# Performance work log

Hardware: AMD Instinct MI355X
Metric: run time of the kernel (lower is better)

The kernel has to match this reference:

```python
import jax, jax.numpy as jnp
import numpy as np

SCALE = 8
NUM_CLASSES = 15
IGNORE_THRES = 0.5
# anchors for scale=8 divided by scale
GRID_ANCHOR = jnp.array([[96.0 / 8, 230.0 / 8], [79.0 / 8, 186.0 / 8], [81.0 / 8, 133.0 / 8]], dtype=jnp.float32)  # [3,2]


def _bce_sum(p, t, mask):
    # torch BCELoss(reduction='sum') with log clamped at -100, restricted to mask
    lp = jnp.maximum(jnp.log(p), -100.0)
    ln = jnp.maximum(jnp.log(1.0 - p), -100.0)
    return jnp.sum(-(t * lp + (1.0 - t) * ln) * mask)


def setup_inputs() -> dict:
    key = jax.random.key(0)
    k1, k2, k3 = jax.random.split(key, 3)
    nB, nG = 128, 52
    x = jax.random.normal(k1, (nB, 3 * (NUM_CLASSES + 5), nG, nG), dtype=jnp.float32)
    boxes = jax.random.uniform(k2, (nB, 4), minval=0.1, maxval=0.6)  # cx,cy,w,h in (0,1)
    cls = jax.random.randint(k3, (nB, 1), 0, NUM_CLASSES).astype(jnp.float32)
    labels = jnp.concatenate([boxes, cls], axis=-1)  # [nB,5]
    return {"x": x, "labels": labels}


def reference(x, labels):
    nB, nG = x.shape[0], x.shape[2]
    pred = x.reshape(nB, 3, NUM_CLASSES + 5, nG, nG).transpose(0, 1, 3, 4, 2)  # [B,3,G,G,20]
    px = jax.nn.sigmoid(pred[..., 0])
    py = jax.nn.sigmoid(pred[..., 1])
    pw = pred[..., 2]
    ph = pred[..., 3]
    conf = jax.nn.sigmoid(pred[..., 4])
    cls = jax.nn.softmax(pred[..., 5:], axis=-1)
    pred_boxs = jnp.stack([px, py, pw, ph], axis=-1)  # [B,3,G,G,4]
    out = jnp.concatenate([
        pred_boxs.reshape(nB, -1, 4) * SCALE,
        conf.reshape(nB, -1, 1),
        cls.reshape(nB, -1, NUM_CLASSES),
    ], axis=-1)

    # ---- build_targets (vectorized; one target per image as in original loop) ----
    tb = labels[:, :4] * nG  # boxes in grid units [B,4]
    gx, gy, gw, gh = tb[:, 0], tb[:, 1], tb[:, 2], tb[:, 3]
    gi = gx.astype(jnp.int32)
    gj = gy.astype(jnp.int32)
    gcls = labels[:, 4].astype(jnp.int32)

    # wh-IoU anchors vs targets -> [3,B]
    aw, ah = GRID_ANCHOR[:, 0:1], GRID_ANCHOR[:, 1:2]
    inter_wh = jnp.minimum(aw, gw[None, :]) * jnp.minimum(ah, gh[None, :])
    ious = inter_wh / (aw * ah + 1e-16 + gw[None, :] * gh[None, :] - inter_wh)
    best_idx = jnp.argmax(ious, axis=0)  # [B]

    bidx = jnp.arange(nB)
    shape4 = (nB, 3, nG, nG)
    obj = jnp.zeros(shape4, jnp.float32).at[bidx, best_idx, gj, gi].set(1.0)

    noobj = jnp.ones(shape4, jnp.float32)
    arep = jnp.tile(jnp.arange(3), nB)
    brep = jnp.repeat(bidx, 3)
    jrep = jnp.repeat(gj, 3)
    irep = jnp.repeat(gi, 3)
    ign = (jnp.reshape(ious.T, (-1,)) > IGNORE_THRES).astype(jnp.float32)
    noobj = noobj.at[brep, arep, jrep, irep].mul(1.0 - ign)
    noobj = noobj.at[bidx, best_idx, gj, gi].set(0.0)

    gif = gi.astype(jnp.float32)
    gjf = gj.astype(jnp.float32)
    tx = jnp.zeros(shape4, jnp.float32).at[bidx, best_idx, gj, gi].set(gx - gif)
    ty = jnp.zeros(shape4, jnp.float32).at[bidx, best_idx, gj, gi].set(gy - gjf)
    tw = jnp.zeros(shape4, jnp.float32).at[bidx, best_idx, gj, gi].set(jnp.log(gw / GRID_ANCHOR[best_idx, 0] + 1e-16))
    th = jnp.zeros(shape4, jnp.float32).at[bidx, best_idx, gj, gi].set(jnp.log(gh / GRID_ANCHOR[best_idx, 1] + 1e-16))
    tcls = jnp.zeros(shape4 + (NUM_CLASSES,), jnp.float32).at[bidx, best_idx, gj, gi, gcls].set(1.0)

    # cls_mask: does argmax of predicted class at target cell match gt class
    pred_cls_at = cls[bidx, best_idx, gj, gi]  # [B,15]
    cls_hit = (jnp.argmax(pred_cls_at, axis=-1) == gcls).astype(jnp.float32)
    cls_mask = jnp.zeros(shape4, jnp.float32).at[bidx, best_idx, gj, gi].set(cls_hit)

    # iou between pred box at target cell and target box (cxcywh, +1 corner convention)
    pb = pred_boxs[bidx, best_idx, gj, gi]  # [B,4]
    b1x1, b1y1 = pb[:, 0] - pb[:, 2] / 2, pb[:, 1] - pb[:, 3] / 2
    b1x2, b1y2 = pb[:, 0] + pb[:, 2] / 2, pb[:, 1] + pb[:, 3] / 2
    b2x1, b2y1 = gx - gw / 2, gy - gh / 2
    b2x2, b2y2 = gx + gw / 2, gy + gh / 2
    iw = jnp.clip(jnp.minimum(b1x2, b2x2) - jnp.maximum(b1x1, b2x1) + 1, 0)
    ih = jnp.clip(jnp.minimum(b1y2, b2y2) - jnp.maximum(b1y1, b2y1) + 1, 0)
    inter = iw * ih
    a1 = (b1x2 - b1x1 + 1) * (b1y2 - b1y1 + 1)
    a2 = (b2x2 - b2x1 + 1) * (b2y2 - b2y1 + 1)
    iou_vec = inter / (a1 + a2 - inter + 1e-16)
    iou_scores = jnp.zeros(shape4, jnp.float32).at[bidx, best_idx, gj, gi].set(iou_vec)

    tconf = obj
    # ---- losses (boolean-mask indexing replaced by masked sums) ----
    loss_x = jnp.sum(jnp.abs(px - tx) * obj)
    loss_y = jnp.sum(jnp.abs(py - ty) * obj)
    loss_w = jnp.sum(jnp.abs(pw - tw) * obj)
    loss_h = jnp.sum(jnp.abs(ph - th) * obj)
    loss_conf = _bce_sum(conf, tconf, obj) + 100.0 * _bce_sum(conf, tconf, noobj)
    loss_cls = _bce_sum(cls, tcls, obj[..., None])
    loss = loss_x + loss_y + loss_w + loss_h + loss_conf + loss_cls
    return (loss, out)
```

## Files before the change

kernel.cpp:

```cpp
#include <hip/hip_runtime.h>
#include <math.h>

#define NB    128
#define NG    52
#define NGG   2704
#define NA    3
#define NCLS  15
#define NCH   20
#define NQ    8112
#define TOTAL 1038336
#define BLK   256
#define CPT   2
#define CPB   (BLK*CPT)
#define NBLK  (TOTAL/CPB)
#define FPB   (CPB*NCH)
#define NQUAD ((FPB-4)/4)

__global__ __launch_bounds__(BLK) void main_kernel(const float* __restrict__ x,
                                                   float* __restrict__ out,
                                                   float* __restrict__ partials) {
    __shared__ __align__(16) float sm[FPB];
    __shared__ float wred[BLK/64];

    int t = threadIdx.x;
    int g = blockIdx.x * BLK + t;
    int cell0 = g * CPT;
    int b  = cell0 / NQ;
    int r  = cell0 - b * NQ;
    int a  = r / NGG;
    int ji = r - a * NGG;

    const float2* __restrict__ xp =
        (const float2*)(x + ((size_t)(b*60 + a*20)) * NGG) + (ji >> 1);

    float za[NCH], zb[NCH];
    #pragma unroll
    for (int c = 0; c < NCH; c++) {
        float2 zz = xp[c * (NGG/2)];
        za[c] = zz.x; zb[c] = zz.y;
    }

    float tsum = 0.0f;
    #pragma unroll
    for (int i = 0; i < CPT; i++) {
        const float* z = (i == 0) ? za : zb;
        float v[NCH];
        float conf = 1.0f / (1.0f + expf(-z[4]));
        v[0] = 8.0f / (1.0f + expf(-z[0]));
        v[1] = 8.0f / (1.0f + expf(-z[1]));
        v[2] = 8.0f * z[2];
        v[3] = 8.0f * z[3];
        v[4] = conf;
        float m = z[5];
        #pragma unroll
        for (int c = 6; c < NCH; c++) m = fmaxf(m, z[c]);
        float s = 0.0f;
        #pragma unroll
        for (int c = 0; c < NCLS; c++) { v[5+c] = expf(z[5+c] - m); s += v[5+c]; }
        float inv = 1.0f / s;
        #pragma unroll
        for (int c = 0; c < NCLS; c++) v[5+c] *= inv;

        tsum += -fmaxf(logf(1.0f - conf), -100.0f);

        int cl = (t * CPT + i);
        int base = cl * NCH - 3;
        #pragma unroll
        for (int c = 0; c < NCH; c++) {
            int L = base + c;
            if (L < 0) L += FPB;
            sm[L] = v[c];
        }
    }

    #pragma unroll
    for (int off = 32; off > 0; off >>= 1) tsum += __shfl_down(tsum, off, 64);
    if ((t & 63) == 0) wred[t >> 6] = tsum;

    __syncthreads();

    size_t gbase = (size_t)blockIdx.x * FPB;
    float4* __restrict__ op = (float4*)(out + gbase + 4);
    const float4* __restrict__ sp = (const float4*)sm;
    #pragma unroll
    for (int k = 0; k < 10; k++) {
        int q = k * BLK + t;
        if (q < NQUAD) op[q] = sp[q];
    }
    if (t == 0) {
        out[gbase + 1]    = sm[FPB - 3];
        out[gbase + 2]    = sm[FPB - 2];
        out[gbase + 3]    = sm[FPB - 1];
        out[gbase + FPB]  = sm[FPB - 4];
        partials[blockIdx.x] = wred[0] + wred[1] + wred[2] + wred[3];
    }
}

__global__ void finish_kernel(const float* __restrict__ labels,
                              const float* __restrict__ partials,
                              float* __restrict__ out) {
    int t = threadIdx.x;
    float s = 0.0f;
    for (int q = t; q < NBLK; q += 256) s += partials[q];

    float corr_part = 0.0f;
    if (t < NB) {
        int b = t;
        float gx = labels[b*5+0] * (float)NG;
        float gy = labels[b*5+1] * (float)NG;
        float gw = labels[b*5+2] * (float)NG;
        float gh = labels[b*5+3] * (float)NG;
        int gcls = (int)labels[b*5+4];
        int gi = (int)gx, gj = (int)gy;
        const float aw[3] = {12.0f, 9.875f, 10.125f};
        const float ah[3] = {28.75f, 23.25f, 16.625f};
        float iou[3];
        #pragma unroll
        for (int a = 0; a < 3; a++) {
            float inter = fminf(aw[a], gw) * fminf(ah[a], gh);
            iou[a] = inter / (aw[a]*ah[a] + 1e-16f + gw*gh - inter);
        }
        int best = 0; float bv = iou[0];
        if (iou[1] > bv) { best = 1; bv = iou[1]; }
        if (iou[2] > bv) { best = 2; bv = iou[2]; }
        float txv = gx - (float)gi;
        float tyv = gy - (float)gj;
        float twv = logf(gw / aw[best] + 1e-16f);
        float thv = logf(gh / ah[best] + 1e-16f);

        float corr = 0.0f;
        #pragma unroll
        for (int a = 0; a < 3; a++) {
            int q = a*NGG + gj*NG + gi;
            const float* ob = out + 1 + ((size_t)b*NQ + q) * NCH;
            float conf = ob[4];
            bool isbest = (a == best);
            if (isbest || iou[a] > 0.5f) {
                corr += -fmaxf(logf(1.0f - conf), -100.0f);
            }
            if (isbest) {
                corr_part += -fmaxf(logf(conf), -100.0f);
                float px = ob[0]*0.125f, py = ob[1]*0.125f;
                float pw = ob[2]*0.125f, ph = ob[3]*0.125f;
                corr_part += fabsf(px - txv) + fabsf(py - tyv)
                           + fabsf(pw - twv) + fabsf(ph - thv);
                for (int c = 0; c < NCLS; c++) {
                    float p = ob[5 + c];
                    if (c == gcls) corr_part += -fmaxf(logf(p),        -100.0f);
                    else           corr_part += -fmaxf(logf(1.0f - p), -100.0f);
                }
            }
        }
        corr_part -= 100.0f * corr;
    }

    __shared__ float red[256];
    red[t] = 100.0f * s + corr_part;
    __syncthreads();
    for (int s2 = 128; s2 > 0; s2 >>= 1) {
        if (t < s2) red[t] += red[t + s2];
        __syncthreads();
    }
    if (t == 0) out[0] = red[0];
}

extern "C" void kernel_launch(void* const* d_in, const int* in_sizes, int n_in,
                              void* d_out, int out_size, void* d_ws, size_t ws_size,
                              hipStream_t stream) {
    const float* x      = (const float*)d_in[0];
    const float* labels = (const float*)d_in[1];
    float* out = (float*)d_out;
    float* ws  = (float*)d_ws;

    hipLaunchKernelGGL(main_kernel,   dim3(NBLK), dim3(BLK), 0, stream, x, out, ws);
    hipLaunchKernelGGL(finish_kernel, dim3(1),    dim3(256), 0, stream, labels, ws, out);
}
```

Measured before the change: 158.7 us.

## Fuse target loss correction into main kernel and use one cell per thread

Moves the per-image target correction (IoU anchor selection, coordinate, class and confidence terms) out of the single-block finish kernel and into the main kernel, where each thread checks whether its cell is the target cell. Each thread now processes one cell instead of two, which doubles the block count, and the output copy uses nontemporal vector stores. This removes the serial tail in the finish kernel that reread the output, but every thread now loads labels and does the IoU arithmetic, and the scalar loads replace the earlier float2 loads.

New measurement: 156.6 us. About the same (-1.3%).

```diff
diff --git a/kernel.cpp b/kernel.cpp
--- a/kernel.cpp
+++ b/kernel.cpp
@@ -10,67 +10,95 @@
 #define NQ    8112
 #define TOTAL 1038336
 #define BLK   256
-#define CPT   2
-#define CPB   (BLK*CPT)
-#define NBLK  (TOTAL/CPB)
-#define FPB   (CPB*NCH)
+#define NBLK  (TOTAL/BLK)
+#define FPB   (BLK*NCH)
 #define NQUAD ((FPB-4)/4)
 
+typedef float f4 __attribute__((ext_vector_type(4)));
+
 __global__ __launch_bounds__(BLK) void main_kernel(const float* __restrict__ x,
+                                                   const float* __restrict__ labels,
                                                    float* __restrict__ out,
                                                    float* __restrict__ partials) {
     __shared__ __align__(16) float sm[FPB];
     __shared__ float wred[BLK/64];
 
     int t = threadIdx.x;
-    int g = blockIdx.x * BLK + t;
-    int cell0 = g * CPT;
-    int b  = cell0 / NQ;
-    int r  = cell0 - b * NQ;
+    int cell = blockIdx.x * BLK + t;
+    int b  = cell / NQ;
+    int r  = cell - b * NQ;
     int a  = r / NGG;
     int ji = r - a * NGG;
 
-    const float2* __restrict__ xp =
-        (const float2*)(x + ((size_t)(b*60 + a*20)) * NGG) + (ji >> 1);
+    const float* __restrict__ xp = x + ((size_t)(b*60 + a*20)) * NGG + ji;
+    float z[NCH];
+    #pragma unroll
+    for (int c = 0; c < NCH; c++) z[c] = xp[c * NGG];
 
-    float za[NCH], zb[NCH];
+    float v[NCH];
+    float conf = 1.0f / (1.0f + expf(-z[4]));
+    v[0] = 8.0f / (1.0f + expf(-z[0]));
+    v[1] = 8.0f / (1.0f + expf(-z[1]));
+    v[2] = 8.0f * z[2];
+    v[3] = 8.0f * z[3];
+    v[4] = conf;
+    float m = z[5];
+    #pragma unroll
+    for (int c = 6; c < NCH; c++) m = fmaxf(m, z[c]);
+    float s = 0.0f;
+    #pragma unroll
+    for (int c = 0; c < NCLS; c++) { v[5+c] = expf(z[5+c] - m); s += v[5+c]; }
+    float inv = 1.0f / s;
+    #pragma unroll
+    for (int c = 0; c < NCLS; c++) v[5+c] *= inv;
+
+    float gx = labels[b*5+0] * (float)NG;
+    float gy = labels[b*5+1] * (float)NG;
+    float gw = labels[b*5+2] * (float)NG;
+    float gh = labels[b*5+3] * (float)NG;
+    int  gcls = (int)labels[b*5+4];
+    int gi = (int)gx, gj = (int)gy;
+    float gwgh = gw * gh;
+    float i0 = fminf(12.0f,   gw) * fminf(28.75f,  gh);
+    float i1 = fminf(9.875f,  gw) * fminf(23.25f,  gh);
+    float i2 = fminf(10.125f, gw) * fminf(16.625f, gh);
+    float iou0 = i0 / (345.0f      + 1e-16f + gwgh - i0);
+    float iou1 = i1 / (229.59375f  + 1e-16f + gwgh - i1);
+    float iou2 = i2 / (168.328125f + 1e-16f + gwgh - i2);
+    int best = 0; float bv = iou0;
+    if (iou1 > bv) { best = 1; bv = iou1; }
+    if (iou2 > bv) { best = 2; bv = iou2; }
+    float ioua = (a == 0) ? iou0 : ((a == 1) ? iou1 : iou2);
+    bool at_t   = (ji == gj * NG + gi);
+    bool isbest = (a == best);
+
+    float tsum = 0.0f;
+    if (!(at_t && (isbest || ioua > 0.5f)))
+        tsum = -100.0f * fmaxf(logf(1.0f - conf), -100.0f);
+    if (at_t && isbest) {
+        tsum += -fmaxf(logf(conf), -100.0f);
+        float txv = gx - (float)gi;
+        float tyv = gy - (float)gj;
+        float abw = (best == 0) ? 12.0f  : ((best == 1) ? 9.875f : 10.125f);
+        float abh = (best == 0) ? 28.75f : ((best == 1) ? 23.25f : 16.625f);
+        float twv = logf(gw / abw + 1e-16f);
+        float thv = logf(gh / abh + 1e-16f);
+        tsum += fabsf(v[0]*0.125f - txv) + fabsf(v[1]*0.125f - tyv)
+              + fabsf(v[2]*0.125f - twv) + fabsf(v[3]*0.125f - thv);
+        #pragma unroll
+        for (int c = 0; c < NCLS; c++) {
+            float p = v[5+c];
+            tsum += (c == gcls) ? -fmaxf(logf(p),        -100.0f)
+                                : -fmaxf(logf(1.0f - p), -100.0f);
+        }
+    }
+
+    int base = t * NCH - 3;
     #pragma unroll
     for (int c = 0; c < NCH; c++) {
-        float2 zz = xp[c * (NGG/2)];
-        za[c] = zz.x; zb[c] = zz.y;
-    }
-
-    float tsum = 0.0f;
-    #pragma unroll
-    for (int i = 0; i < CPT; i++) {
-        const float* z = (i == 0) ? za : zb;
-        float v[NCH];
-        float conf = 1.0f / (1.0f + expf(-z[4]));
-        v[0] = 8.0f / (1.0f + expf(-z[0]));
-        v[1] = 8.0f / (1.0f + expf(-z[1]));
-        v[2] = 8.0f * z[2];
-        v[3] = 8.0f * z[3];
-        v[4] = conf;
-        float m = z[5];
-        #pragma unroll
-        for (int c = 6; c < NCH; c++) m = fmaxf(m, z[c]);
-        float s = 0.0f;
-        #pragma unroll
-        for (int c = 0; c < NCLS; c++) { v[5+c] = expf(z[5+c] - m); s += v[5+c]; }
-        float inv = 1.0f / s;
-        #pragma unroll
-        for (int c = 0; c < NCLS; c++) v[5+c] *= inv;
-
-        tsum += -fmaxf(logf(1.0f - conf), -100.0f);
-
-        int cl = (t * CPT + i);
-        int base = cl * NCH - 3;
-        #pragma unroll
-        for (int c = 0; c < NCH; c++) {
-            int L = base + c;
-            if (L < 0) L += FPB;
-            sm[L] = v[c];
-        }
+        int L = base + c;
+        if (L < 0) L += FPB;
+        sm[L] = v[c];
     }
 
     #pragma unroll
@@ -80,85 +108,32 @@
     __syncthreads();
 
     size_t gbase = (size_t)blockIdx.x * FPB;
-    float4* __restrict__ op = (float4*)(out + gbase + 4);
-    const float4* __restrict__ sp = (const float4*)sm;
+    f4* __restrict__ op = (f4*)(out + gbase + 4);
+    const f4* __restrict__ sp = (const f4*)sm;
     #pragma unroll
-    for (int k = 0; k < 10; k++) {
+    for (int k = 0; k < 5; k++) {
         int q = k * BLK + t;
-        if (q < NQUAD) op[q] = sp[q];
+        if (q < NQUAD) __builtin_nontemporal_store(sp[q], &op[q]);
     }
     if (t == 0) {
-        out[gbase + 1]    = sm[FPB - 3];
-        out[gbase + 2]    = sm[FPB - 2];
-        out[gbase + 3]    = sm[FPB - 1];
-        out[gbase + FPB]  = sm[FPB - 4];
+        out[gbase + 1]   = sm[FPB - 3];
+        out[gbase + 2]   = sm[FPB - 2];
+        out[gbase + 3]   = sm[FPB - 1];
+        out[gbase + FPB] = sm[FPB - 4];
         partials[blockIdx.x] = wred[0] + wred[1] + wred[2] + wred[3];
     }
 }
 
-__global__ void finish_kernel(const float* __restrict__ labels,
-                              const float* __restrict__ partials,
+__global__ void finish_kernel(const float* __restrict__ partials,
                               float* __restrict__ out) {
     int t = threadIdx.x;
     float s = 0.0f;
     for (int q = t; q < NBLK; q += 256) s += partials[q];
-
-    float corr_part = 0.0f;
-    if (t < NB) {
-        int b = t;
-        float gx = labels[b*5+0] * (float)NG;
-        float gy = labels[b*5+1] * (float)NG;
-        float gw = labels[b*5+2] * (float)NG;
-        float gh = labels[b*5+3] * (float)NG;
-        int gcls = (int)labels[b*5+4];
-        int gi = (int)gx, gj = (int)gy;
-        const float aw[3] = {12.0f, 9.875f, 10.125f};
-        const float ah[3] = {28.75f, 23.25f, 16.625f};
-        float iou[3];
-        #pragma unroll
-        for (int a = 0; a < 3; a++) {
-            float inter = fminf(aw[a], gw) * fminf(ah[a], gh);
-            iou[a] = inter / (aw[a]*ah[a] + 1e-16f + gw*gh - inter);
-        }
-        int best = 0; float bv = iou[0];
-        if (iou[1] > bv) { best = 1; bv = iou[1]; }
-        if (iou[2] > bv) { best = 2; bv = iou[2]; }
-        float txv = gx - (float)gi;
-        float tyv = gy - (float)gj;
-        float twv = logf(gw / aw[best] + 1e-16f);
-        float thv = logf(gh / ah[best] + 1e-16f);
-
-        float corr = 0.0f;
-        #pragma unroll
-        for (int a = 0; a < 3; a++) {
-            int q = a*NGG + gj*NG + gi;
-            const float* ob = out + 1 + ((size_t)b*NQ + q) * NCH;
-            float conf = ob[4];
-            bool isbest = (a == best);
-            if (isbest || iou[a] > 0.5f) {
-                corr += -fmaxf(logf(1.0f - conf), -100.0f);
-            }
-            if (isbest) {
-                corr_part += -fmaxf(logf(conf), -100.0f);
-                float px = ob[0]*0.125f, py = ob[1]*0.125f;
-                float pw = ob[2]*0.125f, ph = ob[3]*0.125f;
-                corr_part += fabsf(px - txv) + fabsf(py - tyv)
-                           + fabsf(pw - twv) + fabsf(ph - thv);
-                for (int c = 0; c < NCLS; c++) {
-                    float p = ob[5 + c];
-                    if (c == gcls) corr_part += -fmaxf(logf(p),        -100.0f);
-                    else           corr_part += -fmaxf(logf(1.0f - p), -100.0f);
-                }
-            }
-        }
-        corr_part -= 100.0f * corr;
-    }
-
     __shared__ float red[256];
-    red[t] = 100.0f * s + corr_part;
+    red[t] = s;
     __syncthreads();
-    for (int s2 = 128; s2 > 0; s2 >>= 1) {
-        if (t < s2) red[t] += red[t + s2];
+    for (int k = 128; k > 0; k >>= 1) {
+        if (t < k) red[t] += red[t + k];
         __syncthreads();
     }
     if (t == 0) out[0] = red[0];
@@ -172,6 +147,6 @@
     float* out = (float*)d_out;
     float* ws  = (float*)d_ws;
 
-    hipLaunchKernelGGL(main_kernel,   dim3(NBLK), dim3(BLK), 0, stream, x, out, ws);
-    hipLaunchKernelGGL(finish_kernel, dim3(1),    dim3(256), 0, stream, labels, ws, out);
+    hipLaunchKernelGGL(main_kernel,   dim3(NBLK), dim3(BLK), 0, stream, x, labels, out, ws);
+    hipLaunchKernelGGL(finish_kernel, dim3(1),    dim3(256), 0, stream, ws, out);
 }
```
